# Kernel optimization log

Hardware: AMD Instinct MI355X
Metric: run time of the kernel (lower is better)

## Reference

```python
import jax, jax.numpy as jnp
import numpy as np

HEAD_SIZE = 64
EMBED_DIM = 1024

def setup_inputs() -> dict:
    key = jax.random.key(0)
    kx, kq, kk, kv = jax.random.split(key, 4)
    B, T, C, H = 8, 2048, EMBED_DIM, HEAD_SIZE
    scale = 1.0 / np.sqrt(C)
    x = jax.random.normal(kx, (B, T, C), dtype=jnp.float32)
    # nn.Linear(C, H, bias=False): weight (H, C); store as (C, H) for x @ W
    Wq = jax.random.normal(kq, (C, H), dtype=jnp.float32) * scale
    Wk = jax.random.normal(kk, (C, H), dtype=jnp.float32) * scale
    Wv = jax.random.normal(kv, (C, H), dtype=jnp.float32) * scale
    return {"x": x, "Wq": Wq, "Wk": Wk, "Wv": Wv}

def reference(x, Wq, Wk, Wv):
    B, T, C = x.shape
    H = Wq.shape[1]
    q = x @ Wq  # (B, T, H)
    k = x @ Wk
    v = x @ Wv
    # scaled scores with causal mask (tril)
    wei = jnp.einsum('bth,bsh->bts', q, k) * (H ** -0.5)  # (B, T, T)
    causal = jnp.tril(jnp.ones((T, T), dtype=bool))
    wei = jnp.where(causal, wei, -jnp.inf)
    wei = jax.nn.softmax(wei, axis=-1)
    out = jnp.einsum('bts,bsh->bth', wei, v)  # (B, T, H)
    return out
```

## Files before the change

kernel.cpp:

```cpp
#include <hip/hip_runtime.h>

#define T_SEQ 2048
#define C_DIM 1024
#define H_DIM 64
#define B_DIM 8
#define NROW (B_DIM * T_SEQ)
#define ASTRIDE 44

typedef __attribute__((ext_vector_type(8))) short short8;
typedef __attribute__((ext_vector_type(4))) short short4v;
typedef __attribute__((ext_vector_type(4))) float f32x4;

__device__ __forceinline__ short f2bf(float f) {
  unsigned u = __builtin_bit_cast(unsigned, f);
  u += 0x7fffu + ((u >> 16) & 1u);
  return (short)(u >> 16);
}

union FragU {
  short8 v;
  short4v h[2];
};

__global__ __launch_bounds__(256) void w_transpose(
    const float* __restrict__ Wq, const float* __restrict__ Wk,
    const float* __restrict__ Wv, short* __restrict__ Wt) {
  __shared__ float tile[64][65];
  const int mat = blockIdx.x >> 4;
  const int k0 = (blockIdx.x & 15) * 64;
  const float* W = (mat == 0) ? Wq : (mat == 1 ? Wk : Wv);
  const int t = threadIdx.x;
#pragma unroll
  for (int i = 0; i < 16; ++i) {
    int idx = t + i * 256;
    int kk = idx >> 6, h = idx & 63;
    tile[kk][h] = W[(size_t)(k0 + kk) * H_DIM + h];
  }
  __syncthreads();
#pragma unroll
  for (int i = 0; i < 16; ++i) {
    int idx = t + i * 256;
    int h = idx >> 6, kk = idx & 63;
    Wt[((size_t)mat * 64 + h) * C_DIM + k0 + kk] = f2bf(tile[kk][h]);
  }
}

__global__ __launch_bounds__(256) void qkv_gemm(
    const float* __restrict__ x, const short* __restrict__ Wt,
    short* __restrict__ q, short* __restrict__ k, short* __restrict__ vt) {
  __shared__ __align__(16) short As[64 * ASTRIDE];
  __shared__ __align__(16) short Bs[64 * ASTRIDE];
  const int tid = threadIdx.x;
  const int w = tid >> 6, lane = tid & 63;
  const int n16 = lane & 15, quad = lane >> 4;
  const int cb = blockIdx.x % 3;
  const int rb = blockIdx.x / 3;
  const int row0 = rb * 64;

  const int sr = tid >> 2;
  const int sp = (tid & 3) * 8;
  const float* xg = x + (size_t)(row0 + sr) * C_DIM + sp;
  const short* wg = Wt + ((size_t)cb * 64 + sr) * C_DIM + sp;
  short* asw = As + sr * ASTRIDE + sp;
  short* bsw = Bs + sr * ASTRIDE + sp;

  const short* afp = As + (w * 16 + n16) * ASTRIDE + quad * 8;

  f32x4 acc[4];
#pragma unroll
  for (int i = 0; i < 4; ++i) acc[i] = (f32x4){0.f, 0.f, 0.f, 0.f};

  for (int kc = 0; kc < C_DIM / 32; ++kc) {
    const int k0 = kc * 32;
    const float4 a0 = *(const float4*)(xg + k0);
    const float4 a1 = *(const float4*)(xg + k0 + 4);
    const short8 bw = *(const short8*)(wg + k0);
    __syncthreads();
    short4v wlo, whi;
    wlo[0] = f2bf(a0.x); wlo[1] = f2bf(a0.y);
    wlo[2] = f2bf(a0.z); wlo[3] = f2bf(a0.w);
    whi[0] = f2bf(a1.x); whi[1] = f2bf(a1.y);
    whi[2] = f2bf(a1.z); whi[3] = f2bf(a1.w);
    *(short4v*)asw = wlo;
    *(short4v*)(asw + 4) = whi;
    short4v blo, bhi;
#pragma unroll
    for (int e = 0; e < 4; ++e) { blo[e] = bw[e]; bhi[e] = bw[e + 4]; }
    *(short4v*)bsw = blo;
    *(short4v*)(bsw + 4) = bhi;
    __syncthreads();

    FragU af;
    af.h[0] = *(const short4v*)afp;
    af.h[1] = *(const short4v*)(afp + 4);
#pragma unroll
    for (int nt = 0; nt < 4; ++nt) {
      const short* bp = Bs + (nt * 16 + n16) * ASTRIDE + quad * 8;
      FragU bf;
      bf.h[0] = *(const short4v*)bp;
      bf.h[1] = *(const short4v*)(bp + 4);
      acc[nt] =
          __builtin_amdgcn_mfma_f32_16x16x32_bf16(af.v, bf.v, acc[nt], 0, 0, 0);
    }
  }

  const int gr0 = row0 + w * 16;
  const int b = gr0 >> 11, jr = gr0 & (T_SEQ - 1);
  if (cb == 0) {
#pragma unroll
    for (int nt = 0; nt < 4; ++nt)
#pragma unroll
      for (int r = 0; r < 4; ++r)
        q[(size_t)(gr0 + quad * 4 + r) * H_DIM + nt * 16 + n16] =
            f2bf(acc[nt][r] * 0.125f);
  } else if (cb == 1) {
#pragma unroll
    for (int nt = 0; nt < 4; ++nt)
#pragma unroll
      for (int r = 0; r < 4; ++r)
        k[(size_t)(gr0 + quad * 4 + r) * H_DIM + nt * 16 + n16] =
            f2bf(acc[nt][r]);
  } else {
#pragma unroll
    for (int nt = 0; nt < 4; ++nt)
#pragma unroll
      for (int r = 0; r < 4; ++r)
        vt[((size_t)b * H_DIM + nt * 16 + n16) * T_SEQ + jr + quad * 4 + r] =
            f2bf(acc[nt][r]);
  }
}

__global__ __launch_bounds__(256) void attn_mfma(
    const short* __restrict__ q, const short* __restrict__ k,
    const short* __restrict__ vt, float* __restrict__ out) {
  __shared__ __align__(16) short pbuf[4][1024];
  __shared__ __align__(16) float oshare[3][1024];
  __shared__ __align__(16) float lshare[3][256];
  const int tid = threadIdx.x;
  const int w = tid >> 6;
  const int lane = tid & 63;
  const int n16 = lane & 15, quad = lane >> 4;
  const int b = blockIdx.x & 7;
  const int qt = (T_SEQ / 16 - 1) - (blockIdx.x >> 3);
  const int r0 = qt * 16;

  const short* qb = q + ((size_t)b * T_SEQ + r0) * H_DIM;
  const short* kb = k + (size_t)b * T_SEQ * H_DIM;
  const short* vb = vt + (size_t)b * H_DIM * T_SEQ;

  const short8 aq0 = *(const short8*)(qb + (size_t)n16 * H_DIM + quad * 8);
  const short8 aq1 = *(const short8*)(qb + (size_t)n16 * H_DIM + 32 + quad * 8);

  f32x4 O[4];
#pragma unroll
  for (int i = 0; i < 4; ++i) O[i] = (f32x4){0.f, 0.f, 0.f, 0.f};
  float lsum[4] = {0.f, 0.f, 0.f, 0.f};

  const int nj = (r0 + 16 + 63) >> 6;
  for (int jt = w; jt < nj; jt += 4) {
    const int j0 = jt * 64;

    short8 bk[4][2];
#pragma unroll
    for (int nt = 0; nt < 4; ++nt) {
      const short* kp = kb + (size_t)(j0 + nt * 16 + n16) * H_DIM + quad * 8;
      bk[nt][0] = *(const short8*)kp;
      bk[nt][1] = *(const short8*)(kp + 32);
    }

    f32x4 s[4];
#pragma unroll
    for (int nt = 0; nt < 4; ++nt) {
      f32x4 z = (f32x4){0.f, 0.f, 0.f, 0.f};
      z = __builtin_amdgcn_mfma_f32_16x16x32_bf16(aq0, bk[nt][0], z, 0, 0, 0);
      z = __builtin_amdgcn_mfma_f32_16x16x32_bf16(aq1, bk[nt][1], z, 0, 0, 0);
      s[nt] = z;
    }

    const bool full = (j0 + 64 <= r0);
#pragma unroll
    for (int nt = 0; nt < 4; ++nt) {
      const int base =
          (nt >> 1) * 512 + ((((nt & 1) << 1) | (n16 >> 3)) * 128) + (n16 & 7);
#pragma unroll
      for (int r = 0; r < 4; ++r) {
        float p;
        if (full) {
          p = __expf(s[nt][r]);
        } else {
          const int j = j0 + nt * 16 + n16;
          const int row = r0 + quad * 4 + r;
          p = (j <= row) ? __expf(s[nt][r]) : 0.f;
        }
        lsum[r] += p;
        pbuf[w][base + (quad * 4 + r) * 8] = f2bf(p);
      }
    }

    short8 bv[4][2];
#pragma unroll
    for (int ht = 0; ht < 4; ++ht)
#pragma unroll
      for (int kh = 0; kh < 2; ++kh)
        bv[ht][kh] = *(const short8*)(vb + (size_t)(ht * 16 + n16) * T_SEQ +
                                      j0 + kh * 32 + quad * 8);

    const short8 ap0 = *(const short8*)(&pbuf[w][0] + lane * 8);
    const short8 ap1 = *(const short8*)(&pbuf[w][0] + 512 + lane * 8);

#pragma unroll
    for (int ht = 0; ht < 4; ++ht) {
      O[ht] = __builtin_amdgcn_mfma_f32_16x16x32_bf16(ap0, bv[ht][0], O[ht], 0, 0, 0);
      O[ht] = __builtin_amdgcn_mfma_f32_16x16x32_bf16(ap1, bv[ht][1], O[ht], 0, 0, 0);
    }
  }

  if (w != 0) {
#pragma unroll
    for (int ht = 0; ht < 4; ++ht)
#pragma unroll
      for (int r = 0; r < 4; ++r)
        oshare[w - 1][(ht * 4 + r) * 64 + lane] = O[ht][r];
#pragma unroll
    for (int r = 0; r < 4; ++r) lshare[w - 1][r * 64 + lane] = lsum[r];
  }
  __syncthreads();
  if (w == 0) {
#pragma unroll
    for (int ht = 0; ht < 4; ++ht)
#pragma unroll
      for (int r = 0; r < 4; ++r) {
        float a = O[ht][r];
#pragma unroll
        for (int ow = 0; ow < 3; ++ow) a += oshare[ow][(ht * 4 + r) * 64 + lane];
        O[ht][r] = a;
      }
#pragma unroll
    for (int r = 0; r < 4; ++r) {
      float vsum = lsum[r];
#pragma unroll
      for (int ow = 0; ow < 3; ++ow) vsum += lshare[ow][r * 64 + lane];
      vsum += __shfl_xor(vsum, 1);
      vsum += __shfl_xor(vsum, 2);
      vsum += __shfl_xor(vsum, 4);
      vsum += __shfl_xor(vsum, 8);
      lsum[r] = vsum;
    }
#pragma unroll
    for (int ht = 0; ht < 4; ++ht)
#pragma unroll
      for (int r = 0; r < 4; ++r)
        out[((size_t)b * T_SEQ + r0 + quad * 4 + r) * H_DIM + ht * 16 + n16] =
            O[ht][r] / lsum[r];
  }
}

extern "C" void kernel_launch(void* const* d_in, const int* in_sizes, int n_in,
                              void* d_out, int out_size, void* d_ws,
                              size_t ws_size, hipStream_t stream) {
  const float* x = (const float*)d_in[0];
  const float* Wq = (const float*)d_in[1];
  const float* Wk = (const float*)d_in[2];
  const float* Wv = (const float*)d_in[3];

  char* ws = (char*)d_ws;
  short* Wt = (short*)ws;
  short* q = (short*)(ws + 3 * 64 * 1024 * 2);
  short* kk = (short*)(ws + 3 * 64 * 1024 * 2 + 2097152);
  short* vt = (short*)(ws + 3 * 64 * 1024 * 2 + 2 * 2097152);

  w_transpose<<<48, 256, 0, stream>>>(Wq, Wk, Wv, Wt);
  qkv_gemm<<<3 * (NROW / 64), 256, 0, stream>>>(x, Wt, q, kk, vt);
  attn_mfma<<<B_DIM * (T_SEQ / 16), 256, 0, stream>>>(q, kk, vt, (float*)d_out);
}
```

Baseline: 161.6 us.

## Restructure QKV GEMM to compute all 192 columns per block, reading x once

Each QKV GEMM block now handles 32 rows and all three Q/K/V output column groups, so x is read from global memory once instead of three times. Weights are staged into LDS with direct global-to-LDS loads using an XOR swizzle to avoid bank conflicts. x fragments are loaded straight into registers and converted to bf16, with no LDS staging, over 128-wide K chunks. This cuts the dominant x traffic, but uses a 48KB LDS tile and leaves no overlap between the weight loads and the MFMA work.

After: 168.7 us. 4.4% more time.

```diff
diff --git a/kernel.cpp b/kernel.cpp
--- a/kernel.cpp
+++ b/kernel.cpp
@@ -5,10 +5,8 @@
 #define H_DIM 64
 #define B_DIM 8
 #define NROW (B_DIM * T_SEQ)
-#define ASTRIDE 44
 
 typedef __attribute__((ext_vector_type(8))) short short8;
-typedef __attribute__((ext_vector_type(4))) short short4v;
 typedef __attribute__((ext_vector_type(4))) float f32x4;
 
 __device__ __forceinline__ short f2bf(float f) {
@@ -17,10 +15,11 @@
   return (short)(u >> 16);
 }
 
-union FragU {
-  short8 v;
-  short4v h[2];
-};
+__device__ __forceinline__ void gll16(const void* g, void* l) {
+  __builtin_amdgcn_global_load_lds(
+      (const __attribute__((address_space(1))) unsigned int*)g,
+      (__attribute__((address_space(3))) unsigned int*)l, 16, 0, 0);
+}
 
 __global__ __launch_bounds__(256) void w_transpose(
     const float* __restrict__ Wq, const float* __restrict__ Wk,
@@ -48,86 +47,85 @@
 __global__ __launch_bounds__(256) void qkv_gemm(
     const float* __restrict__ x, const short* __restrict__ Wt,
     short* __restrict__ q, short* __restrict__ k, short* __restrict__ vt) {
-  __shared__ __align__(16) short As[64 * ASTRIDE];
-  __shared__ __align__(16) short Bs[64 * ASTRIDE];
+  __shared__ __align__(16) short Bs[192 * 128];
   const int tid = threadIdx.x;
   const int w = tid >> 6, lane = tid & 63;
   const int n16 = lane & 15, quad = lane >> 4;
-  const int cb = blockIdx.x % 3;
-  const int rb = blockIdx.x / 3;
-  const int row0 = rb * 64;
-
-  const int sr = tid >> 2;
-  const int sp = (tid & 3) * 8;
-  const float* xg = x + (size_t)(row0 + sr) * C_DIM + sp;
-  const short* wg = Wt + ((size_t)cb * 64 + sr) * C_DIM + sp;
-  short* asw = As + sr * ASTRIDE + sp;
-  short* bsw = Bs + sr * ASTRIDE + sp;
-
-  const short* afp = As + (w * 16 + n16) * ASTRIDE + quad * 8;
-
-  f32x4 acc[4];
-#pragma unroll
-  for (int i = 0; i < 4; ++i) acc[i] = (f32x4){0.f, 0.f, 0.f, 0.f};
-
-  for (int kc = 0; kc < C_DIM / 32; ++kc) {
-    const int k0 = kc * 32;
-    const float4 a0 = *(const float4*)(xg + k0);
-    const float4 a1 = *(const float4*)(xg + k0 + 4);
-    const short8 bw = *(const short8*)(wg + k0);
+  const int row0 = blockIdx.x * 32;
+
+  f32x4 acc[2][3];
+#pragma unroll
+  for (int mt = 0; mt < 2; ++mt)
+#pragma unroll
+    for (int nt = 0; nt < 3; ++nt) acc[mt][nt] = (f32x4){0.f, 0.f, 0.f, 0.f};
+
+  for (int kc = 0; kc < 8; ++kc) {
+    const int k0 = kc * 128;
     __syncthreads();
-    short4v wlo, whi;
-    wlo[0] = f2bf(a0.x); wlo[1] = f2bf(a0.y);
-    wlo[2] = f2bf(a0.z); wlo[3] = f2bf(a0.w);
-    whi[0] = f2bf(a1.x); whi[1] = f2bf(a1.y);
-    whi[2] = f2bf(a1.z); whi[3] = f2bf(a1.w);
-    *(short4v*)asw = wlo;
-    *(short4v*)(asw + 4) = whi;
-    short4v blo, bhi;
-#pragma unroll
-    for (int e = 0; e < 4; ++e) { blo[e] = bw[e]; bhi[e] = bw[e + 4]; }
-    *(short4v*)bsw = blo;
-    *(short4v*)(bsw + 4) = bhi;
+#pragma unroll
+    for (int i = 0; i < 12; ++i) {
+      const int du = w * 768 + i * 64;
+      const int d = du + lane;
+      const int h = d >> 4, up = d & 15;
+      const int ul = up ^ (h & 7);
+      gll16(Wt + (size_t)h * C_DIM + k0 + ul * 8, (char*)Bs + (size_t)du * 16);
+    }
+    float4 a[2][4][2];
+#pragma unroll
+    for (int mt = 0; mt < 2; ++mt)
+#pragma unroll
+      for (int kh = 0; kh < 4; ++kh) {
+        const float* ap = x + (size_t)(row0 + mt * 16 + n16) * C_DIM + k0 +
+                          kh * 32 + quad * 8;
+        a[mt][kh][0] = *(const float4*)ap;
+        a[mt][kh][1] = *(const float4*)(ap + 4);
+      }
     __syncthreads();
 
-    FragU af;
-    af.h[0] = *(const short4v*)afp;
-    af.h[1] = *(const short4v*)(afp + 4);
-#pragma unroll
-    for (int nt = 0; nt < 4; ++nt) {
-      const short* bp = Bs + (nt * 16 + n16) * ASTRIDE + quad * 8;
-      FragU bf;
-      bf.h[0] = *(const short4v*)bp;
-      bf.h[1] = *(const short4v*)(bp + 4);
-      acc[nt] =
-          __builtin_amdgcn_mfma_f32_16x16x32_bf16(af.v, bf.v, acc[nt], 0, 0, 0);
-    }
-  }
-
-  const int gr0 = row0 + w * 16;
-  const int b = gr0 >> 11, jr = gr0 & (T_SEQ - 1);
-  if (cb == 0) {
-#pragma unroll
-    for (int nt = 0; nt < 4; ++nt)
-#pragma unroll
-      for (int r = 0; r < 4; ++r)
-        q[(size_t)(gr0 + quad * 4 + r) * H_DIM + nt * 16 + n16] =
-            f2bf(acc[nt][r] * 0.125f);
-  } else if (cb == 1) {
-#pragma unroll
-    for (int nt = 0; nt < 4; ++nt)
-#pragma unroll
-      for (int r = 0; r < 4; ++r)
-        k[(size_t)(gr0 + quad * 4 + r) * H_DIM + nt * 16 + n16] =
-            f2bf(acc[nt][r]);
-  } else {
-#pragma unroll
-    for (int nt = 0; nt < 4; ++nt)
-#pragma unroll
-      for (int r = 0; r < 4; ++r)
-        vt[((size_t)b * H_DIM + nt * 16 + n16) * T_SEQ + jr + quad * 4 + r] =
-            f2bf(acc[nt][r]);
-  }
+    short8 af[2][4];
+#pragma unroll
+    for (int mt = 0; mt < 2; ++mt)
+#pragma unroll
+      for (int kh = 0; kh < 4; ++kh) {
+#pragma unroll
+        for (int e = 0; e < 4; ++e) {
+          af[mt][kh][e] = f2bf(((const float*)&a[mt][kh][0])[e]);
+          af[mt][kh][e + 4] = f2bf(((const float*)&a[mt][kh][1])[e]);
+        }
+      }
+#pragma unroll
+    for (int kh = 0; kh < 4; ++kh)
+#pragma unroll
+      for (int nt = 0; nt < 3; ++nt) {
+        const int h = w * 48 + nt * 16 + n16;
+        const int up = (kh * 4 + quad) ^ (h & 7);
+        const short8 bf = *(const short8*)(Bs + (size_t)h * 128 + up * 8);
+        acc[0][nt] =
+            __builtin_amdgcn_mfma_f32_16x16x32_bf16(af[0][kh], bf, acc[0][nt], 0, 0, 0);
+        acc[1][nt] =
+            __builtin_amdgcn_mfma_f32_16x16x32_bf16(af[1][kh], bf, acc[1][nt], 0, 0, 0);
+      }
+  }
+
+  const int b = row0 >> 11;
+#pragma unroll
+  for (int mt = 0; mt < 2; ++mt)
+#pragma unroll
+    for (int nt = 0; nt < 3; ++nt) {
+      const int c = w * 48 + nt * 16 + n16;
+      const int mat = c >> 6, cl = c & 63;
+#pragma unroll
+      for (int r = 0; r < 4; ++r) {
+        const int row = row0 + mt * 16 + quad * 4 + r;
+        const float v = acc[mt][nt][r];
+        if (mat == 0)
+          q[(size_t)row * H_DIM + cl] = f2bf(v * 0.125f);
+        else if (mat == 1)
+          k[(size_t)row * H_DIM + cl] = f2bf(v);
+        else
+          vt[((size_t)b * H_DIM + cl) * T_SEQ + (row & (T_SEQ - 1))] = f2bf(v);
+      }
+    }
 }
 
 __global__ __launch_bounds__(256) void attn_mfma(
@@ -270,6 +268,6 @@
   short* vt = (short*)(ws + 3 * 64 * 1024 * 2 + 2 * 2097152);
 
   w_transpose<<<48, 256, 0, stream>>>(Wq, Wk, Wv, Wt);
-  qkv_gemm<<<3 * (NROW / 64), 256, 0, stream>>>(x, Wt, q, kk, vt);
+  qkv_gemm<<<NROW / 32, 256, 0, stream>>>(x, Wt, q, kk, vt);
   attn_mfma<<<B_DIM * (T_SEQ / 16), 256, 0, stream>>>(q, kk, vt, (float*)d_out);
 }
```
